# Performance work log

Hardware: AMD Instinct MI355X
Metric: run time of the kernel (lower is better)

## Reference

```python
import jax, jax.numpy as jnp
import numpy as np

B, T, V, E, H = 1024, 256, 90, 8, 256


def setup_inputs() -> dict:
    key = jax.random.key(0)
    ks = jax.random.split(key, 40)
    rn = lambda k, shape: jax.random.normal(k, shape, dtype=jnp.float32) * 0.05
    inp = {}
    inp["input_seq"] = jax.random.randint(ks[0], (B, T), 0, V, dtype=jnp.int32)
    inp["emb"] = rn(ks[1], (V, E)).at[0].set(0.0)  # padding_idx=0
    i = 2
    for name, din in [("g1", E), ("g2", H), ("l1", E), ("l2", H)]:
        inp[name + "_Wih"] = rn(ks[i], (4 * H, din)); i += 1
        inp[name + "_Whh"] = rn(ks[i], (4 * H, H)); i += 1
        inp[name + "_bih"] = rn(ks[i], (4 * H,)); i += 1
        inp[name + "_bhh"] = rn(ks[i], (4 * H,)); i += 1
    for name in ["p1", "p2"]:
        inp[name + "_W1"] = rn(ks[i], (2 * H, E + 4 * H)); i += 1
        inp[name + "_b1"] = rn(ks[i], (2 * H,)); i += 1
        inp[name + "_W2"] = rn(ks[i], (H, 2 * H)); i += 1
        inp[name + "_b2"] = rn(ks[i], (H,)); i += 1
        inp[name + "_W3"] = rn(ks[i], (2, H)); i += 1
        inp[name + "_b3"] = rn(ks[i], (2,)); i += 1
    inp["gfc_W"] = rn(ks[i], (V, H)); i += 1
    inp["gfc_b"] = rn(ks[i], (V,)); i += 1
    inp["lfc_W"] = rn(ks[i], (V, H)); i += 1
    inp["lfc_b"] = rn(ks[i], (V,))
    return inp


def _cell(x, h, c, Wih, Whh, bih, bhh):
    # PyTorch LSTMCell: gate order i, f, g, o
    g = x @ Wih.T + h @ Whh.T + (bih + bhh)
    i, f, gg, o = jnp.split(g, 4, axis=-1)
    c = jax.nn.sigmoid(f) * c + jax.nn.sigmoid(i) * jnp.tanh(gg)
    return jax.nn.sigmoid(o) * jnp.tanh(c), c


def _mlp(x, W1, b1, W2, b2, W3, b3):
    h = jax.nn.relu(x @ W1.T + b1)
    h = jax.nn.relu(h @ W2.T + b2)
    return h @ W3.T + b3


def _forward(input_seq, emb,
             g1_Wih, g1_Whh, g1_bih, g1_bhh, g2_Wih, g2_Whh, g2_bih, g2_bhh,
             l1_Wih, l1_Whh, l1_bih, l1_bhh, l2_Wih, l2_Whh, l2_bih, l2_bhh,
             p1_W1, p1_b1, p1_W2, p1_b2, p1_W3, p1_b3,
             p2_W1, p2_b1, p2_W2, p2_b2, p2_W3, p2_b3,
             gfc_W, gfc_b, lfc_W, lfc_b):
    Bn = input_seq.shape[0]
    embeds = emb[input_seq]  # [B, T, E]
    z = jnp.zeros((Bn, H), dtype=emb.dtype)

    def step(carry, e):
        gh1, gc1, gh2, gc2, lh1, lc1, lh2, lc2 = carry
        gh1, gc1 = _cell(e, gh1, gc1, g1_Wih, g1_Whh, g1_bih, g1_bhh)
        lh1, lc1 = _cell(e, lh1, lc1, l1_Wih, l1_Whh, l1_bih, l1_bhh)
        p = jax.nn.softmax(_mlp(jnp.concatenate([e, gh1, gc1, lh1, lc1], 1),
                                p1_W1, p1_b1, p1_W2, p1_b2, p1_W3, p1_b3), axis=1)
        # bmm([B,1,2],[B,2,H]) == p0*local + p1*global
        gh1 = p[:, 0:1] * lh1 + p[:, 1:2] * gh1
        gc1 = p[:, 0:1] * lc1 + p[:, 1:2] * gc1
        gh2, gc2 = _cell(gh1, gh2, gc2, g2_Wih, g2_Whh, g2_bih, g2_bhh)
        lh2, lc2 = _cell(lh1, lh2, lc2, l2_Wih, l2_Whh, l2_bih, l2_bhh)
        p = jax.nn.softmax(_mlp(jnp.concatenate([e, gh2, gc2, lh2, lc2], 1),
                                p2_W1, p2_b1, p2_W2, p2_b2, p2_W3, p2_b3), axis=1)
        gh2 = p[:, 0:1] * lh2 + p[:, 1:2] * gh2
        gc2 = p[:, 0:1] * lc2 + p[:, 1:2] * gc2
        return (gh1, gc1, gh2, gc2, lh1, lc1, lh2, lc2), gh2

    _, hs = jax.lax.scan(step, (z, z, z, z, z, z, z, z), jnp.swapaxes(embeds, 0, 1))
    hs = jnp.swapaxes(hs, 0, 1)  # [B, T, H]
    out = 0.5 * (hs @ gfc_W.T + gfc_b) + 0.5 * (hs @ lfc_W.T + lfc_b)
    return jnp.swapaxes(out, 1, 2)  # [B, V, T]


def reference(input_seq, emb,
              g1_Wih, g1_Whh, g1_bih, g1_bhh, g2_Wih, g2_Whh, g2_bih, g2_bhh,
              l1_Wih, l1_Whh, l1_bih, l1_bhh, l2_Wih, l2_Whh, l2_bih, l2_bhh,
              p1_W1, p1_b1, p1_W2, p1_b2, p1_W3, p1_b3,
              p2_W1, p2_b1, p2_W2, p2_b2, p2_W3, p2_b3,
              gfc_W, gfc_b, lfc_W, lfc_b):
    return _forward(input_seq, emb,
                    g1_Wih, g1_Whh, g1_bih, g1_bhh, g2_Wih, g2_Whh, g2_bih, g2_bhh,
                    l1_Wih, l1_Whh, l1_bih, l1_bhh, l2_Wih, l2_Whh, l2_bih, l2_bhh,
                    p1_W1, p1_b1, p1_W2, p1_b2, p1_W3, p1_b3,
                    p2_W1, p2_b1, p2_W2, p2_b2, p2_W3, p2_b3,
                    gfc_W, gfc_b, lfc_W, lfc_b)
```

## Files before the change

kernel.cpp:

```cpp
#include <hip/hip_runtime.h>

#define B_ 1024
#define T_ 256
#define V_ 90
#define H_ 256
#define NTHR 512
#define NBLK 256
#define S_ (B_*H_)

constexpr size_t OFF_GH1C = 0;
constexpr size_t OFF_GC1C = OFF_GH1C + S_;
constexpr size_t OFF_GH1P = OFF_GC1C + S_;
constexpr size_t OFF_GC1P = OFF_GH1P + S_;
constexpr size_t OFF_LH1  = OFF_GC1P + S_;
constexpr size_t OFF_LC1  = OFF_LH1 + 2*S_;
constexpr size_t OFF_GH2C = OFF_LC1 + 2*S_;
constexpr size_t OFF_GC2C = OFF_GH2C + S_;
constexpr size_t OFF_GH2P = OFF_GC2C + S_;
constexpr size_t OFF_GC2P = OFF_GH2P + S_;
constexpr size_t OFF_LH2  = OFF_GC2P + S_;
constexpr size_t OFF_LC2  = OFF_LH2 + 2*S_;
constexpr size_t OFF_MLP1 = OFF_LC2 + 2*S_;
constexpr size_t OFF_EX   = OFF_MLP1 + (size_t)B_*512;
constexpr size_t OFF_WG1  = OFF_EX + 2*B_*8;
constexpr size_t OFF_WE1  = OFF_WG1 + 256*2048;
constexpr size_t OFF_BG1  = OFF_WE1 + 8*2048;
constexpr size_t OFF_WL2  = OFF_BG1 + 2048;
constexpr size_t OFF_BL2  = OFF_WL2 + 512*1024;
constexpr size_t OFF_WG2  = OFF_BL2 + 1024;
constexpr size_t OFF_BG2  = OFF_WG2 + 512*1024;
constexpr size_t OFF_WP1  = OFF_BG2 + 1024;
constexpr size_t OFF_WEP1 = OFF_WP1 + 1024*512;
constexpr size_t OFF_WP2  = OFF_WEP1 + 8*512;
constexpr size_t OFF_WEP2 = OFF_WP2 + 1024*512;
constexpr size_t OFF_WB1  = OFF_WEP2 + 8*512;
constexpr size_t OFF_WB2  = OFF_WB1 + 512*256;
constexpr size_t OFF_WOUT = OFF_WB2 + 512*256;
constexpr size_t OFF_BOUT = OFF_WOUT + 256*96;
constexpr size_t OFF_BAR  = OFF_BOUT + 112;
constexpr size_t WS_FLOATS = OFF_BAR + 8192;

struct InP {
  const int*   seq;
  const float* emb;
  const float *g1_Wih,*g1_Whh,*g1_bih,*g1_bhh;
  const float *g2_Wih,*g2_Whh,*g2_bih,*g2_bhh;
  const float *l1_Wih,*l1_Whh,*l1_bih,*l1_bhh;
  const float *l2_Wih,*l2_Whh,*l2_bih,*l2_bhh;
  const float *p1_W1,*p1_b1,*p1_W2,*p1_b2,*p1_W3,*p1_b3;
  const float *p2_W1,*p2_b1,*p2_W2,*p2_b2,*p2_W3,*p2_b3;
  const float *gfc_W,*gfc_b,*lfc_W,*lfc_b;
};

__device__ __forceinline__ float sig_(float x)  { return 1.f/(1.f+__expf(-x)); }
__device__ __forceinline__ float tanh_(float x) { return 1.f - 2.f/(__expf(2.f*x)+1.f); }

__device__ __forceinline__ unsigned ld_flag(const unsigned* p) {
  unsigned v;
  asm volatile("global_load_dword %0, %1, off sc1\n\ts_waitcnt vmcnt(0)"
               : "=v"(v) : "v"(p) : "memory");
  return v;
}
__device__ __forceinline__ void st_flag(unsigned* p, unsigned v) {
  asm volatile("global_store_dword %0, %1, off sc1\n\ts_waitcnt vmcnt(0)"
               :: "v"(p), "v"(v) : "memory");
}

__device__ __forceinline__ void gbar_x(unsigned* arr, unsigned* go, int slot, unsigned ep)
{
  __syncthreads();
  if (threadIdx.x < 64) {
    if (threadIdx.x == 0) st_flag(&arr[slot*16], ep);
    if (slot == 0) {
      if (threadIdx.x < 32) {
        int cap = 0;
        for (;;) {
          unsigned v = ld_flag(&arr[threadIdx.x*16]);
          if (v >= ep) break;
          __builtin_amdgcn_s_sleep(2);
          if (++cap > 65536) break;
        }
      }
      if (threadIdx.x == 0) st_flag(go, ep);
    } else if (threadIdx.x == 0) {
      int cap = 0;
      for (;;) {
        unsigned v = ld_flag(go);
        if (v >= ep) break;
        __builtin_amdgcn_s_sleep(2);
        if (++cap > 65536) break;
      }
    }
  }
  __syncthreads();
  asm volatile("buffer_inv sc0" ::: "memory");
}

template<int CT, int TR, int NSEG, bool HASE, class FE>
__device__ __forceinline__ void mm_tile(
    float* sAb, float* sWb, float* sWe, float* sE,
    const float* s0, const float* s1_, const float* s2_, const float* s3_,
    const float* Wm, int ldw, int ct0,
    const float* We, int ldwe, const float* ex,
    int r0, FE fe)
{
  constexpr int NTX = CT / 4;
  constexpr int LDW = CT + 4;
  constexpr int K   = NSEG * 256;
  constexpr int NC  = K / 32;
  constexpr int WPT = (32*CT)/NTHR;
  const int tid = threadIdx.x;
  const int tx = tid % NTX, ty = tid / NTX;
  const int ar = tid >> 3, ak = (tid & 7) << 2;
  const int kkw = tid >> 4, cw = (tid & 15) * WPT;

  if (HASE) {
    for (int i = tid; i < 8*CT; i += NTHR) {
      int kk = i / CT, c = i - kk*CT;
      sWe[kk*LDW + c] = We[(size_t)kk*ldwe + ct0 + c];
    }
    sE[tid] = ex[((r0 + (tid>>3))<<3) + (tid & 7)];
  }

  float acc[TR][4];
#pragma unroll
  for (int i = 0; i < TR; ++i)
#pragma unroll
    for (int j = 0; j < 4; ++j) acc[i][j] = 0.f;

  auto lda = [&](int k0) -> float4 {
    const float* S;
    if (NSEG == 1) S = s0;
    else if (NSEG == 2) S = (k0 < 256) ? s0 : s1_;
    else S = (k0 < 256) ? s0 : (k0 < 512) ? s1_ : (k0 < 768) ? s2_ : s3_;
    return *(const float4*)&S[(size_t)(r0 + ar)*H_ + (k0 & 255) + ak];
  };
  auto ldwv0 = [&](int k0) { return *(const float4*)&Wm[(size_t)(k0 + kkw)*ldw + ct0 + cw]; };
  auto ldwv1 = [&](int k0) { return *(const float4*)&Wm[(size_t)(k0 + kkw)*ldw + ct0 + cw + 4]; };

  auto storec = [&](int pb, const float4& pa, const float4& pw0, const float4& pw1) {
    float* a = sAb + pb*2176;
    a[(ak+0)*68 + ar] = pa.x; a[(ak+1)*68 + ar] = pa.y;
    a[(ak+2)*68 + ar] = pa.z; a[(ak+3)*68 + ar] = pa.w;
    float* w = sWb + pb*4224 + kkw*LDW + cw;
    *(float4*)w = pw0;
    if (WPT == 8) *(float4*)(w+4) = pw1;
  };

  auto compute = [&](const float* a, const float* w) {
#pragma unroll 8
    for (int kk = 0; kk < 32; ++kk) {
      float4 wv = *(const float4*)&w[kk*LDW + tx*4];
      if constexpr (TR == 4) {
        float4 av = *(const float4*)&a[kk*68 + ty*4];
        float avv[4] = {av.x, av.y, av.z, av.w};
#pragma unroll
        for (int i = 0; i < 4; ++i) {
          acc[i][0] = __builtin_fmaf(avv[i], wv.x, acc[i][0]);
          acc[i][1] = __builtin_fmaf(avv[i], wv.y, acc[i][1]);
          acc[i][2] = __builtin_fmaf(avv[i], wv.z, acc[i][2]);
          acc[i][3] = __builtin_fmaf(avv[i], wv.w, acc[i][3]);
        }
      } else {
        float2 av = *(const float2*)&a[kk*68 + ty*2];
        float avv[2] = {av.x, av.y};
#pragma unroll
        for (int i = 0; i < 2; ++i) {
          acc[i][0] = __builtin_fmaf(avv[i], wv.x, acc[i][0]);
          acc[i][1] = __builtin_fmaf(avv[i], wv.y, acc[i][1]);
          acc[i][2] = __builtin_fmaf(avv[i], wv.z, acc[i][2]);
          acc[i][3] = __builtin_fmaf(avv[i], wv.w, acc[i][3]);
        }
      }
    }
  };

  float4 pa0, pw00, pw01, pa1, pw10, pw11;
  pa0 = lda(0);  pw00 = ldwv0(0);  if (WPT == 8) pw01 = ldwv1(0);
  pa1 = lda(32); pw10 = ldwv0(32); if (WPT == 8) pw11 = ldwv1(32);
  storec(0, pa0, pw00, pw01);
  __syncthreads();

  for (int c = 0; c < NC; c += 2) {
    if (c + 2 < NC) { pa0 = lda((c+2)*32); pw00 = ldwv0((c+2)*32); if (WPT == 8) pw01 = ldwv1((c+2)*32); }
    compute(sAb, sWb);
    storec(1, pa1, pw10, pw11);
    __syncthreads();
    if (c + 3 < NC) { pa1 = lda((c+3)*32); pw10 = ldwv0((c+3)*32); if (WPT == 8) pw11 = ldwv1((c+3)*32); }
    compute(sAb + 2176, sWb + 4224);
    if (c + 2 < NC) storec(0, pa0, pw00, pw01);
    __syncthreads();
  }

  if (HASE) {
#pragma unroll
    for (int j = 0; j < 8; ++j) {
      float4 wv = *(const float4*)&sWe[j*LDW + tx*4];
#pragma unroll
      for (int i = 0; i < TR; ++i) {
        float ev = sE[(ty*TR + i)*8 + j];
        acc[i][0] = __builtin_fmaf(ev, wv.x, acc[i][0]);
        acc[i][1] = __builtin_fmaf(ev, wv.y, acc[i][1]);
        acc[i][2] = __builtin_fmaf(ev, wv.z, acc[i][2]);
        acc[i][3] = __builtin_fmaf(ev, wv.w, acc[i][3]);
      }
    }
  }
  fe(tx, ty, acc);
}

__device__ __forceinline__ void stage_F2(
    int rowbase,
    const float* mlp1, const float* WB, const float* b2,
    const float* W3, const float* b3,
    const float* lh, const float* lc,
    const float* ghp, const float* gcp,
    float* ghc, float* gcc)
{
  const int w = threadIdx.x >> 6, lane = threadIdx.x & 63;
  const int r0 = rowbase + w*2;
  const float* a0 = mlp1 + (size_t)r0*512;
  const float* a1 = a0 + 512;
  float m0[4] = {0.f,0.f,0.f,0.f}, m1[4] = {0.f,0.f,0.f,0.f};
  for (int k0 = 0; k0 < 512; k0 += 4) {
    float4 x0 = *(const float4*)&a0[k0];
    float4 x1 = *(const float4*)&a1[k0];
    float xv0[4] = {x0.x,x0.y,x0.z,x0.w};
    float xv1[4] = {x1.x,x1.y,x1.z,x1.w};
#pragma unroll
    for (int j = 0; j < 4; ++j) {
      float4 wv = *(const float4*)&WB[(size_t)(k0+j)*256 + lane*4];
      m0[0] = __builtin_fmaf(xv0[j], wv.x, m0[0]);
      m0[1] = __builtin_fmaf(xv0[j], wv.y, m0[1]);
      m0[2] = __builtin_fmaf(xv0[j], wv.z, m0[2]);
      m0[3] = __builtin_fmaf(xv0[j], wv.w, m0[3]);
      m1[0] = __builtin_fmaf(xv1[j], wv.x, m1[0]);
      m1[1] = __builtin_fmaf(xv1[j], wv.y, m1[1]);
      m1[2] = __builtin_fmaf(xv1[j], wv.z, m1[2]);
      m1[3] = __builtin_fmaf(xv1[j], wv.w, m1[3]);
    }
  }
  float4 b = *(const float4*)&b2[lane*4];
  float bb[4] = {b.x,b.y,b.z,b.w};
#pragma unroll
  for (int j = 0; j < 4; ++j) {
    m0[j] = fmaxf(m0[j]+bb[j], 0.f);
    m1[j] = fmaxf(m1[j]+bb[j], 0.f);
  }
  float4 w30 = *(const float4*)&W3[lane*4];
  float4 w31 = *(const float4*)&W3[256 + lane*4];
  float w0v[4] = {w30.x,w30.y,w30.z,w30.w};
  float w1v[4] = {w31.x,w31.y,w31.z,w31.w};
  float d00=0.f, d01=0.f, d10=0.f, d11=0.f;
#pragma unroll
  for (int j = 0; j < 4; ++j) {
    d00 = __builtin_fmaf(m0[j], w0v[j], d00);
    d01 = __builtin_fmaf(m0[j], w1v[j], d01);
    d10 = __builtin_fmaf(m1[j], w0v[j], d10);
    d11 = __builtin_fmaf(m1[j], w1v[j], d11);
  }
#pragma unroll
  for (int off = 32; off; off >>= 1) {
    d00 += __shfl_xor(d00, off, 64); d01 += __shfl_xor(d01, off, 64);
    d10 += __shfl_xor(d10, off, 64); d11 += __shfl_xor(d11, off, 64);
  }
  d00 += b3[0]; d01 += b3[1]; d10 += b3[0]; d11 += b3[1];
  float mxa = fmaxf(d00, d01), mxb = fmaxf(d10, d11);
  float e00 = __expf(d00-mxa), e01 = __expf(d01-mxa);
  float e10 = __expf(d10-mxb), e11 = __expf(d11-mxb);
  float ia = 1.f/(e00+e01), ib = 1.f/(e10+e11);
  float p0a = e00*ia, p1a = e01*ia;
  float p0b = e10*ib, p1b = e11*ib;
#pragma unroll
  for (int rr = 0; rr < 2; ++rr) {
    const float p0 = rr ? p0b : p0a, p1 = rr ? p1b : p1a;
    const size_t ix = (size_t)(r0+rr)*H_ + lane*4;
    float4 lv = *(const float4*)&lh[ix];
    float4 gv = *(const float4*)&ghp[ix];
    float4 o;
    o.x = p0*lv.x + p1*gv.x; o.y = p0*lv.y + p1*gv.y;
    o.z = p0*lv.z + p1*gv.z; o.w = p0*lv.w + p1*gv.w;
    *(float4*)&ghc[ix] = o;
    lv = *(const float4*)&lc[ix];
    gv = *(const float4*)&gcp[ix];
    o.x = p0*lv.x + p1*gv.x; o.y = p0*lv.y + p1*gv.y;
    o.z = p0*lv.z + p1*gv.z; o.w = p0*lv.w + p1*gv.w;
    *(float4*)&gcc[ix] = o;
  }
}

__device__ __forceinline__ void stage_OUT(
    const float* gh2c, const float* WOUT, const float* BOUT,
    float* out, int rbase, int tt)
{
  const int w = threadIdx.x >> 6, lane = threadIdx.x & 63;
  const int r = rbase + w;
  const float* arow = gh2c + (size_t)r * H_;
  float acc0 = 0.f, acc1 = 0.f;
  const bool two = lane < (V_ - 64);
  for (int k0 = 0; k0 < 256; k0 += 4) {
    float4 a4 = *(const float4*)&arow[k0];
    float av[4] = {a4.x, a4.y, a4.z, a4.w};
#pragma unroll
    for (int j = 0; j < 4; ++j) {
      const float* wr = &WOUT[(size_t)(k0+j)*96];
      acc0 = __builtin_fmaf(av[j], wr[lane], acc0);
      if (two) acc1 = __builtin_fmaf(av[j], wr[64+lane], acc1);
    }
  }
  out[((size_t)r*V_ + lane)*T_ + tt] = acc0 + BOUT[lane];
  if (two) out[((size_t)r*V_ + 64 + lane)*T_ + tt] = acc1 + BOUT[64+lane];
}

template<int TR>
struct GateEpi {
  const float* cin; float* ho; float* co; const float* bias; int r0; int hbase;
  __device__ void operator()(int tx, int ty, float (&acc)[TR][4]) const {
    const int h = hbase + tx;
    const float b0 = bias[tx*4+0], b1 = bias[tx*4+1];
    const float b2 = bias[tx*4+2], b3 = bias[tx*4+3];
#pragma unroll
    for (int i = 0; i < TR; ++i) {
      const int r = r0 + ty*TR + i;
      const size_t ix = (size_t)r*H_ + h;
      float gi = sig_(acc[i][0]+b0), gf = sig_(acc[i][1]+b1);
      float gg = tanh_(acc[i][2]+b2), go = sig_(acc[i][3]+b3);
      float cn = gf*cin[ix] + gi*gg;
      ho[ix] = go*tanh_(cn); co[ix] = cn;
    }
  }
};

struct MlpEpi {
  float* mlp1; const float* b1; int r0; int c0;
  __device__ void operator()(int tx, int ty, float (&acc)[2][4]) const {
    const float4 b = *(const float4*)&b1[c0 + tx*4];
#pragma unroll
    for (int i = 0; i < 2; ++i) {
      const int r = r0 + ty*2 + i;
      float4 o;
      o.x = fmaxf(acc[i][0]+b.x, 0.f); o.y = fmaxf(acc[i][1]+b.y, 0.f);
      o.z = fmaxf(acc[i][2]+b.z, 0.f); o.w = fmaxf(acc[i][3]+b.w, 0.f);
      *(float4*)&mlp1[(size_t)r*512 + c0 + tx*4] = o;
    }
  }
};

__global__ void k_setup(InP in, float* __restrict__ ws)
{
  const size_t nthr = (size_t)gridDim.x * blockDim.x;
  const size_t t0 = (size_t)blockIdx.x * blockDim.x + threadIdx.x;

  for (size_t i = t0; i < 16*(size_t)S_; i += nthr) ws[i] = 0.f;
  for (size_t i = t0; i < 8192; i += nthr) ((unsigned*)(ws + OFF_BAR))[i] = 0u;

  for (size_t i = t0; i < (size_t)B_*8; i += nthr) {
    int r = (int)(i >> 3), j = (int)(i & 7);
    ws[OFF_EX + i] = in.emb[(size_t)in.seq[(size_t)r*T_]*8 + j];
  }
  for (size_t i = t0; i < (size_t)256*2048; i += nthr) {
    int k = (int)(i >> 11), n = (int)(i & 2047);
    int cell = n >> 10, nn = n & 1023, h = nn >> 2, g = nn & 3, row = g*256 + h;
    const float* W = cell ? in.l1_Whh : in.g1_Whh;
    ws[OFF_WG1 + i] = W[(size_t)row*256 + k];
  }
  for (size_t i = t0; i < (size_t)8*2048; i += nthr) {
    int k = (int)(i >> 11), n = (int)(i & 2047);
    int cell = n >> 10, nn = n & 1023, h = nn >> 2, g = nn & 3, row = g*256 + h;
    const float* W = cell ? in.l1_Wih : in.g1_Wih;
    ws[OFF_WE1 + i] = W[(size_t)row*8 + k];
  }
  for (size_t i = t0; i < 2048; i += nthr) {
    int cell = (int)(i >> 10), nn = (int)(i & 1023), h = nn >> 2, g = nn & 3, row = g*256 + h;
    ws[OFF_BG1 + i] = cell ? (in.l1_bih[row] + in.l1_bhh[row]) : (in.g1_bih[row] + in.g1_bhh[row]);
  }
  for (size_t i = t0; i < (size_t)2*512*1024; i += nthr) {
    int cell = (int)(i / (512*1024));
    int idx = (int)(i - (size_t)cell*512*1024);
    int k = idx >> 10, n = idx & 1023, h = n >> 2, g = n & 3, row = g*256 + h;
    const float* Wih = cell ? in.l2_Wih : in.g2_Wih;
    const float* Whh = cell ? in.l2_Whh : in.g2_Whh;
    float v = (k < 256) ? Wih[(size_t)row*256 + k] : Whh[(size_t)row*256 + (k-256)];
    ws[(cell ? OFF_WL2 : OFF_WG2) + idx] = v;
  }
  for (size_t i = t0; i < 2048; i += nthr) {
    int cell = (int)(i >> 10), n = (int)(i & 1023), h = n >> 2, g = n & 3, row = g*256 + h;
    float v = cell ? (in.l2_bih[row] + in.l2_bhh[row]) : (in.g2_bih[row] + in.g2_bhh[row]);
    ws[(cell ? OFF_BL2 : OFF_BG2) + n] = v;
  }
  for (size_t i = t0; i < (size_t)2*1024*512; i += nthr) {
    int which = (int)(i / (1024*512));
    int idx = (int)(i - (size_t)which*1024*512);
    int k = idx >> 9, n = idx & 511;
    const float* W = which ? in.p2_W1 : in.p1_W1;
    ws[(which ? OFF_WP2 : OFF_WP1) + idx] = W[(size_t)n*1032 + 8 + k];
  }
  for (size_t i = t0; i < (size_t)2*8*512; i += nthr) {
    int which = (int)(i / (8*512));
    int idx = (int)(i - (size_t)which*8*512);
    int k = idx >> 9, n = idx & 511;
    const float* W = which ? in.p2_W1 : in.p1_W1;
    ws[(which ? OFF_WEP2 : OFF_WEP1) + idx] = W[(size_t)n*1032 + k];
  }
  for (size_t i = t0; i < (size_t)2*512*256; i += nthr) {
    int which = (int)(i / (512*256));
    int idx = (int)(i - (size_t)which*512*256);
    int k = idx >> 8, n = idx & 255;
    const float* W = which ? in.p2_W2 : in.p1_W2;
    ws[(which ? OFF_WB2 : OFF_WB1) + idx] = W[(size_t)n*512 + k];
  }
  for (size_t i = t0; i < (size_t)256*96; i += nthr) {
    int k = (int)(i / 96), c = (int)(i - (size_t)k*96);
    float v = 0.f;
    if (c < V_) v = 0.5f*(in.gfc_W[(size_t)c*256 + k] + in.lfc_W[(size_t)c*256 + k]);
    ws[OFF_WOUT + i] = v;
  }
  for (size_t i = t0; i < 96; i += nthr)
    ws[OFF_BOUT + i] = (i < V_) ? 0.5f*(in.gfc_b[i] + in.lfc_b[i]) : 0.f;
}

__global__ __launch_bounds__(NTHR) void k_main(InP in, float* ws, float* __restrict__ out)
{
  __shared__ __attribute__((aligned(16))) float sA[2*2176];
  __shared__ __attribute__((aligned(16))) float sW[2*4224];
  __shared__ __attribute__((aligned(16))) float sWe[8*132];
  __shared__ __attribute__((aligned(16))) float sE[512];

  float* GH1C = ws + OFF_GH1C;  float* GC1C = ws + OFF_GC1C;
  float* GH1P = ws + OFF_GH1P;  float* GC1P = ws + OFF_GC1P;
  float* LH1  = ws + OFF_LH1;   float* LC1  = ws + OFF_LC1;
  float* GH2C = ws + OFF_GH2C;  float* GC2C = ws + OFF_GC2C;
  float* GH2P = ws + OFF_GH2P;  float* GC2P = ws + OFF_GC2P;
  float* LH2  = ws + OFF_LH2;   float* LC2  = ws + OFF_LC2;
  float* MLP1 = ws + OFF_MLP1;  float* EXB  = ws + OFF_EX;
  const float* WG1 = ws + OFF_WG1;  const float* WE1 = ws + OFF_WE1;  const float* BG1 = ws + OFF_BG1;
  const float* WL2 = ws + OFF_WL2;  const float* BL2 = ws + OFF_BL2;
  const float* WG2 = ws + OFF_WG2;  const float* BG2 = ws + OFF_BG2;
  const float* WP1 = ws + OFF_WP1;  const float* WEP1 = ws + OFF_WEP1;
  const float* WP2 = ws + OFF_WP2;  const float* WEP2 = ws + OFF_WEP2;
  const float* WB1 = ws + OFF_WB1;  const float* WB2 = ws + OFF_WB2;
  const float* WOUT = ws + OFF_WOUT; const float* BOUT = ws + OFF_BOUT;

  unsigned xcc;
  asm volatile("s_getreg_b32 %0, hwreg(HW_REG_XCC_ID)" : "=s"(xcc));
  xcc &= 7u;
  unsigned* barx = ((unsigned*)(ws + OFF_BAR)) + xcc*1024;
  unsigned* arr  = barx;
  unsigned* go   = barx + 512;
  unsigned* reg  = barx + 544;
  __shared__ unsigned s_slot;
  if (threadIdx.x == 0)
    s_slot = __hip_atomic_fetch_add(reg, 1u, __ATOMIC_RELAXED, __HIP_MEMORY_SCOPE_AGENT);
  __syncthreads();
  const int slot  = (int)(s_slot & 31u);
  const int rows0 = (int)xcc * 128;
  unsigned ep = 0;

  for (int t = 0; t < T_; ++t) {
    const int sel = t & 1;
    const float* ex = EXB + sel*(B_*8);
    float* lh1o = LH1 + sel*S_;      float* lh1n = LH1 + (sel^1)*S_;
    float* lc1o = LC1 + sel*S_;      float* lc1n = LC1 + (sel^1)*S_;
    float* lh2o = LH2 + sel*S_;      float* lh2n = LH2 + (sel^1)*S_;
    float* lc2o = LC2 + sel*S_;      float* lc2n = LC2 + (sel^1)*S_;

    {
      const int rt = slot & 1, ct = slot >> 1;
      const int r0 = rows0 + rt*64, ct0 = ct*128;
      const int cell = ct >> 3;
      GateEpi<4> epi{ cell ? lc1o : GC1C,
                      cell ? lh1n : GH1P,
                      cell ? lc1n : GC1P,
                      BG1 + ct0, r0, (ct0 & 1023) >> 2 };
      mm_tile<128,4,1,true>(sA, sW, sWe, sE,
                            cell ? lh1o : GH1C, nullptr, nullptr, nullptr,
                            WG1, 2048, ct0, WE1, 2048, ex, r0, epi);
    }
    gbar_x(arr, go, slot, ++ep);

    if (slot < 16) {
      const int rt = slot & 1, ct = slot >> 1;
      const int r0 = rows0 + rt*64, c0 = ct*64;
      MlpEpi epi{ MLP1, in.p1_b1, r0, c0 };
      mm_tile<64,2,4,true>(sA, sW, sWe, sE,
                           GH1P, GC1P, lh1n, lc1n,
                           WP1, 512, c0, WEP1, 512, ex, r0, epi);
    } else {
      const int s2 = slot - 16;
      const int rt = s2 & 1, ct = s2 >> 1;
      const int r0 = rows0 + rt*64, ct0 = ct*128;
      GateEpi<4> epi{ lc2o, lh2n, lc2n, BL2 + ct0, r0, ct0 >> 2 };
      mm_tile<128,4,2,false>(sA, sW, sWe, sE,
                             lh1n, lh2o, nullptr, nullptr,
                             WL2, 1024, ct0, nullptr, 0, nullptr, r0, epi);
    }
    gbar_x(arr, go, slot, ++ep);

    if (slot < 8) {
      stage_F2(rows0 + slot*16, MLP1, WB1, in.p1_b2, in.p1_W3, in.p1_b3,
               lh1n, lc1n, GH1P, GC1P, GH1C, GC1C);
    } else if (slot < 10 && t < T_-1) {
      const int rb = rows0 + (slot-8)*64;
      const int r = rb + (threadIdx.x >> 3), j = threadIdx.x & 7;
      EXB[((t+1)&1)*(B_*8) + r*8 + j] = in.emb[(size_t)in.seq[(size_t)r*T_ + t + 1]*8 + j];
    }
    gbar_x(arr, go, slot, ++ep);

    {
      const int rt = slot & 1, ct = slot >> 1;
      const int r0 = rows0 + rt*64, ct0 = ct*64;
      GateEpi<2> epi{ GC2C, GH2P, GC2P, BG2 + ct0, r0, ct0 >> 2 };
      mm_tile<64,2,2,false>(sA, sW, sWe, sE,
                            GH1C, GH2C, nullptr, nullptr,
                            WG2, 1024, ct0, nullptr, 0, nullptr, r0, epi);
    }
    gbar_x(arr, go, slot, ++ep);

    if (slot < 16) {
      const int rt = slot & 1, ct = slot >> 1;
      const int r0 = rows0 + rt*64, c0 = ct*64;
      MlpEpi epi{ MLP1, in.p2_b1, r0, c0 };
      mm_tile<64,2,4,true>(sA, sW, sWe, sE,
                           GH2P, GC2P, lh2n, lc2n,
                           WP2, 512, c0, WEP2, 512, ex, r0, epi);
    } else if (t > 0) {
      stage_OUT(GH2C, WOUT, BOUT, out, rows0 + (slot-16)*8, t-1);
    }
    gbar_x(arr, go, slot, ++ep);

    if (slot < 8) {
      stage_F2(rows0 + slot*16, MLP1, WB2, in.p2_b2, in.p2_W3, in.p2_b3,
               lh2n, lc2n, GH2P, GC2P, GH2C, GC2C);
    }
    gbar_x(arr, go, slot, ++ep);
  }

  if (slot >= 16) stage_OUT(GH2C, WOUT, BOUT, out, rows0 + (slot-16)*8, 255);
}

extern "C" void kernel_launch(void* const* d_in, const int* in_sizes, int n_in,
                              void* d_out, int out_size, void* d_ws, size_t ws_size,
                              hipStream_t stream)
{
  if (ws_size < WS_FLOATS * sizeof(float)) return;

  InP in;
  in.seq    = (const int*)  d_in[0];
  in.emb    = (const float*)d_in[1];
  in.g1_Wih = (const float*)d_in[2];  in.g1_Whh = (const float*)d_in[3];
  in.g1_bih = (const float*)d_in[4];  in.g1_bhh = (const float*)d_in[5];
  in.g2_Wih = (const float*)d_in[6];  in.g2_Whh = (const float*)d_in[7];
  in.g2_bih = (const float*)d_in[8];  in.g2_bhh = (const float*)d_in[9];
  in.l1_Wih = (const float*)d_in[10]; in.l1_Whh = (const float*)d_in[11];
  in.l1_bih = (const float*)d_in[12]; in.l1_bhh = (const float*)d_in[13];
  in.l2_Wih = (const float*)d_in[14]; in.l2_Whh = (const float*)d_in[15];
  in.l2_bih = (const float*)d_in[16]; in.l2_bhh = (const float*)d_in[17];
  in.p1_W1  = (const float*)d_in[18]; in.p1_b1  = (const float*)d_in[19];
  in.p1_W2  = (const float*)d_in[20]; in.p1_b2  = (const float*)d_in[21];
  in.p1_W3  = (const float*)d_in[22]; in.p1_b3  = (const float*)d_in[23];
  in.p2_W1  = (const float*)d_in[24]; in.p2_b1  = (const float*)d_in[25];
  in.p2_W2  = (const float*)d_in[26]; in.p2_b2  = (const float*)d_in[27];
  in.p2_W3  = (const float*)d_in[28]; in.p2_b3  = (const float*)d_in[29];
  in.gfc_W  = (const float*)d_in[30]; in.gfc_b  = (const float*)d_in[31];
  in.lfc_W  = (const float*)d_in[32]; in.lfc_b  = (const float*)d_in[33];

  float* ws  = (float*)d_ws;
  float* out = (float*)d_out;

  k_setup<<<256, 256, 0, stream>>>(in, ws);
  k_main <<<NBLK, NTHR, 28672, stream>>>(in, ws, out);
}
```

Before: 64.14 ms.

## Replace scalar FP32 GEMM tiles with split-bf16 MFMA matmuls

Replaces the FMA-based shared-memory GEMM tiles in the persistent LSTM kernel with MFMA 16x16x32 bf16 instructions. Each operand is split into high and low bf16 parts and three products are summed to keep roughly FP32 accuracy. Weights are pre-packed into MFMA fragment layout in setup. The MLP first layer is split across K into two partial buffers, with bias and ReLU moved into stage_F2, and the G2 gate matmul tiling is reshaped to 128-column tiles. This trades extra MFMA work and conversion overhead for much higher matrix throughput, with some risk of precision loss.

Measured after the change: 81.34 ms. 26.8% more time.

```diff
diff --git a/kernel.cpp b/kernel.cpp
--- a/kernel.cpp
+++ b/kernel.cpp
@@ -1,4 +1,5 @@
 #include <hip/hip_runtime.h>
+#include <hip/hip_bf16.h>
 
 #define B_ 1024
 #define T_ 256
@@ -8,36 +9,43 @@
 #define NBLK 256
 #define S_ (B_*H_)
 
-constexpr size_t OFF_GH1C = 0;
-constexpr size_t OFF_GC1C = OFF_GH1C + S_;
-constexpr size_t OFF_GH1P = OFF_GC1C + S_;
-constexpr size_t OFF_GC1P = OFF_GH1P + S_;
-constexpr size_t OFF_LH1  = OFF_GC1P + S_;
-constexpr size_t OFF_LC1  = OFF_LH1 + 2*S_;
-constexpr size_t OFF_GH2C = OFF_LC1 + 2*S_;
-constexpr size_t OFF_GC2C = OFF_GH2C + S_;
-constexpr size_t OFF_GH2P = OFF_GC2C + S_;
-constexpr size_t OFF_GC2P = OFF_GH2P + S_;
-constexpr size_t OFF_LH2  = OFF_GC2P + S_;
-constexpr size_t OFF_LC2  = OFF_LH2 + 2*S_;
-constexpr size_t OFF_MLP1 = OFF_LC2 + 2*S_;
-constexpr size_t OFF_EX   = OFF_MLP1 + (size_t)B_*512;
-constexpr size_t OFF_WG1  = OFF_EX + 2*B_*8;
-constexpr size_t OFF_WE1  = OFF_WG1 + 256*2048;
-constexpr size_t OFF_BG1  = OFF_WE1 + 8*2048;
-constexpr size_t OFF_WL2  = OFF_BG1 + 2048;
-constexpr size_t OFF_BL2  = OFF_WL2 + 512*1024;
-constexpr size_t OFF_WG2  = OFF_BL2 + 1024;
-constexpr size_t OFF_BG2  = OFF_WG2 + 512*1024;
-constexpr size_t OFF_WP1  = OFF_BG2 + 1024;
-constexpr size_t OFF_WEP1 = OFF_WP1 + 1024*512;
-constexpr size_t OFF_WP2  = OFF_WEP1 + 8*512;
-constexpr size_t OFF_WEP2 = OFF_WP2 + 1024*512;
-constexpr size_t OFF_WB1  = OFF_WEP2 + 8*512;
-constexpr size_t OFF_WB2  = OFF_WB1 + 512*256;
-constexpr size_t OFF_WOUT = OFF_WB2 + 512*256;
-constexpr size_t OFF_BOUT = OFF_WOUT + 256*96;
-constexpr size_t OFF_BAR  = OFF_BOUT + 112;
+typedef unsigned short u16;
+typedef __attribute__((ext_vector_type(8))) short bf16x8;
+typedef __attribute__((ext_vector_type(4))) float f32x4;
+typedef __attribute__((ext_vector_type(4))) unsigned short u16x4;
+
+constexpr size_t OFF_GH1C  = 0;
+constexpr size_t OFF_GC1C  = OFF_GH1C + S_;
+constexpr size_t OFF_GH1P  = OFF_GC1C + S_;
+constexpr size_t OFF_GC1P  = OFF_GH1P + S_;
+constexpr size_t OFF_LH1   = OFF_GC1P + S_;
+constexpr size_t OFF_LC1   = OFF_LH1 + 2*S_;
+constexpr size_t OFF_GH2C  = OFF_LC1 + 2*S_;
+constexpr size_t OFF_GC2C  = OFF_GH2C + S_;
+constexpr size_t OFF_GH2P  = OFF_GC2C + S_;
+constexpr size_t OFF_GC2P  = OFF_GH2P + S_;
+constexpr size_t OFF_LH2   = OFF_GC2P + S_;
+constexpr size_t OFF_LC2   = OFF_LH2 + 2*S_;
+constexpr size_t OFF_MLP1A = OFF_LC2 + 2*S_;
+constexpr size_t OFF_MLP1B = OFF_MLP1A + (size_t)B_*512;
+constexpr size_t OFF_EX    = OFF_MLP1B + (size_t)B_*512;
+constexpr size_t OFF_WG1PK = OFF_EX + 2*B_*8;
+constexpr size_t OFF_WE1   = OFF_WG1PK + 256*2048/1*1;
+constexpr size_t OFF_WE1_  = OFF_WG1PK + (size_t)256*2048;
+constexpr size_t OFF_BG1   = OFF_WE1_ + 8*2048;
+constexpr size_t OFF_WL2PK = OFF_BG1 + 2048;
+constexpr size_t OFF_BL2   = OFF_WL2PK + (size_t)512*1024;
+constexpr size_t OFF_WG2PK = OFF_BL2 + 1024;
+constexpr size_t OFF_BG2   = OFF_WG2PK + (size_t)512*1024;
+constexpr size_t OFF_WP1PK = OFF_BG2 + 1024;
+constexpr size_t OFF_WEP1  = OFF_WP1PK + (size_t)1024*512;
+constexpr size_t OFF_WP2PK = OFF_WEP1 + 8*512;
+constexpr size_t OFF_WEP2  = OFF_WP2PK + (size_t)1024*512;
+constexpr size_t OFF_WB1   = OFF_WEP2 + 8*512;
+constexpr size_t OFF_WB2   = OFF_WB1 + 512*256;
+constexpr size_t OFF_WOUT  = OFF_WB2 + 512*256;
+constexpr size_t OFF_BOUT  = OFF_WOUT + 256*96;
+constexpr size_t OFF_BAR   = OFF_BOUT + 128;
 constexpr size_t WS_FLOATS = OFF_BAR + 8192;
 
 struct InP {
@@ -54,6 +62,15 @@
 
 __device__ __forceinline__ float sig_(float x)  { return 1.f/(1.f+__expf(-x)); }
 __device__ __forceinline__ float tanh_(float x) { return 1.f - 2.f/(__expf(2.f*x)+1.f); }
+
+__device__ __forceinline__ unsigned short f2bf(float v) {
+  unsigned u = __builtin_bit_cast(unsigned, v);
+  u += 0x7FFFu + ((u >> 16) & 1u);
+  return (unsigned short)(u >> 16);
+}
+__device__ __forceinline__ float bf2f(unsigned short s) {
+  unsigned u = (unsigned)s << 16; return __builtin_bit_cast(float, u);
+}
 
 __device__ __forceinline__ unsigned ld_flag(const unsigned* p) {
   unsigned v;
@@ -96,122 +113,144 @@
   asm volatile("buffer_inv sc0" ::: "memory");
 }
 
-template<int CT, int TR, int NSEG, bool HASE, class FE>
-__device__ __forceinline__ void mm_tile(
-    float* sAb, float* sWb, float* sWe, float* sE,
-    const float* s0, const float* s1_, const float* s2_, const float* s3_,
-    const float* Wm, int ldw, int ct0,
-    const float* We, int ldwe, const float* ex,
-    int r0, FE fe)
+template<int NCH, int NSEG, bool HASE, class FE>
+__device__ __forceinline__ void mm_mfma(
+    u16* sAB, float* sWe, float* sE,
+    const float* s0, const float* s1_,
+    const u16* Wpk, int wstep,
+    const float* WeP, int ldwe, const float* ex,
+    int r0, int ct0, FE fe)
 {
-  constexpr int NTX = CT / 4;
-  constexpr int LDW = CT + 4;
-  constexpr int K   = NSEG * 256;
-  constexpr int NC  = K / 32;
-  constexpr int WPT = (32*CT)/NTHR;
+  constexpr int BUFU = 12288;
   const int tid = threadIdx.x;
-  const int tx = tid % NTX, ty = tid / NTX;
+  const int lane = tid & 63;
+  const int wr = (tid >> 6) & 3, wc = tid >> 8;
   const int ar = tid >> 3, ak = (tid & 7) << 2;
-  const int kkw = tid >> 4, cw = (tid & 15) * WPT;
 
   if (HASE) {
-    for (int i = tid; i < 8*CT; i += NTHR) {
-      int kk = i / CT, c = i - kk*CT;
-      sWe[kk*LDW + c] = We[(size_t)kk*ldwe + ct0 + c];
-    }
-    sE[tid] = ex[((r0 + (tid>>3))<<3) + (tid & 7)];
-  }
-
-  float acc[TR][4];
-#pragma unroll
-  for (int i = 0; i < TR; ++i)
-#pragma unroll
-    for (int j = 0; j < 4; ++j) acc[i][j] = 0.f;
-
-  auto lda = [&](int k0) -> float4 {
-    const float* S;
-    if (NSEG == 1) S = s0;
-    else if (NSEG == 2) S = (k0 < 256) ? s0 : s1_;
-    else S = (k0 < 256) ? s0 : (k0 < 512) ? s1_ : (k0 < 768) ? s2_ : s3_;
-    return *(const float4*)&S[(size_t)(r0 + ar)*H_ + (k0 & 255) + ak];
+    for (int i = tid; i < 8*128; i += NTHR)
+      sWe[i] = WeP[(i >> 7) * ldwe + ct0 + (i & 127)];
+    sE[tid] = ex[((r0 + ar) << 3) + (tid & 7)];
+  }
+
+  f32x4 acc[4] = {{0,0,0,0},{0,0,0,0},{0,0,0,0},{0,0,0,0}};
+
+  auto lda = [&](int c) -> float4 {
+    int k0 = c * 32;
+    const float* S = (NSEG == 1) ? s0 : ((k0 < 256) ? s0 : s1_);
+    return *(const float4*)&S[(size_t)(r0 + ar) * H_ + (k0 & 255) + ak];
   };
-  auto ldwv0 = [&](int k0) { return *(const float4*)&Wm[(size_t)(k0 + kkw)*ldw + ct0 + cw]; };
-  auto ldwv1 = [&](int k0) { return *(const float4*)&Wm[(size_t)(k0 + kkw)*ldw + ct0 + cw + 4]; };
-
-  auto storec = [&](int pb, const float4& pa, const float4& pw0, const float4& pw1) {
-    float* a = sAb + pb*2176;
-    a[(ak+0)*68 + ar] = pa.x; a[(ak+1)*68 + ar] = pa.y;
-    a[(ak+2)*68 + ar] = pa.z; a[(ak+3)*68 + ar] = pa.w;
-    float* w = sWb + pb*4224 + kkw*LDW + cw;
-    *(float4*)w = pw0;
-    if (WPT == 8) *(float4*)(w+4) = pw1;
+  auto ldw = [&](int c, float4& w0, float4& w1) {
+    const float* p = (const float*)(Wpk + (size_t)c * wstep) + tid * 8;
+    w0 = *(const float4*)p; w1 = *(const float4*)(p + 4);
   };
-
-  auto compute = [&](const float* a, const float* w) {
-#pragma unroll 8
-    for (int kk = 0; kk < 32; ++kk) {
-      float4 wv = *(const float4*)&w[kk*LDW + tx*4];
-      if constexpr (TR == 4) {
-        float4 av = *(const float4*)&a[kk*68 + ty*4];
-        float avv[4] = {av.x, av.y, av.z, av.w};
-#pragma unroll
-        for (int i = 0; i < 4; ++i) {
-          acc[i][0] = __builtin_fmaf(avv[i], wv.x, acc[i][0]);
-          acc[i][1] = __builtin_fmaf(avv[i], wv.y, acc[i][1]);
-          acc[i][2] = __builtin_fmaf(avv[i], wv.z, acc[i][2]);
-          acc[i][3] = __builtin_fmaf(avv[i], wv.w, acc[i][3]);
-        }
-      } else {
-        float2 av = *(const float2*)&a[kk*68 + ty*2];
-        float avv[2] = {av.x, av.y};
-#pragma unroll
-        for (int i = 0; i < 2; ++i) {
-          acc[i][0] = __builtin_fmaf(avv[i], wv.x, acc[i][0]);
-          acc[i][1] = __builtin_fmaf(avv[i], wv.y, acc[i][1]);
-          acc[i][2] = __builtin_fmaf(avv[i], wv.z, acc[i][2]);
-          acc[i][3] = __builtin_fmaf(avv[i], wv.w, acc[i][3]);
-        }
-      }
-    }
+  auto storec = [&](int pb, const float4& pa, const float4& w0, const float4& w1) {
+    float vv[4] = {pa.x, pa.y, pa.z, pa.w};
+    u16x4 hv, lv;
+#pragma unroll
+    for (int j = 0; j < 4; ++j) {
+      unsigned short hb = f2bf(vv[j]);
+      hv[j] = hb;
+      lv[j] = f2bf(vv[j] - bf2f(hb));
+    }
+    u16* base = sAB + pb*BUFU;
+    const int aoff = (ar >> 4)*512 + ((ar & 15) + ((ak >> 3) << 4))*8 + (ak & 7);
+    *(u16x4*)(base + aoff) = hv;
+    *(u16x4*)(base + 2048 + aoff) = lv;
+    float* wb = (float*)(base + 4096) + tid*8;
+    *(float4*)wb = w0; *(float4*)(wb + 4) = w1;
   };
-
-  float4 pa0, pw00, pw01, pa1, pw10, pw11;
-  pa0 = lda(0);  pw00 = ldwv0(0);  if (WPT == 8) pw01 = ldwv1(0);
-  pa1 = lda(32); pw10 = ldwv0(32); if (WPT == 8) pw11 = ldwv1(32);
+  auto compute = [&](int pb) {
+    u16* base = sAB + pb*BUFU;
+    const u16* Ap = base + wr*512 + lane*8;
+    bf16x8 a_hi = *(const bf16x8*)Ap;
+    bf16x8 a_lo = *(const bf16x8*)(Ap + 2048);
+    const u16* Bp = base + 4096 + (wc*4)*1024 + lane*8;
+#pragma unroll
+    for (int t = 0; t < 4; ++t) {
+      bf16x8 b_hi = *(const bf16x8*)(Bp + t*1024);
+      bf16x8 b_lo = *(const bf16x8*)(Bp + t*1024 + 512);
+      acc[t] = __builtin_amdgcn_mfma_f32_16x16x32_bf16(a_hi, b_hi, acc[t], 0, 0, 0);
+      acc[t] = __builtin_amdgcn_mfma_f32_16x16x32_bf16(a_lo, b_hi, acc[t], 0, 0, 0);
+      acc[t] = __builtin_amdgcn_mfma_f32_16x16x32_bf16(a_hi, b_lo, acc[t], 0, 0, 0);
+    }
+  };
+
+  float4 pa0, pa1, pw00, pw01, pw10, pw11;
+  pa0 = lda(0); ldw(0, pw00, pw01);
+  pa1 = lda(1); ldw(1, pw10, pw11);
   storec(0, pa0, pw00, pw01);
   __syncthreads();
-
-  for (int c = 0; c < NC; c += 2) {
-    if (c + 2 < NC) { pa0 = lda((c+2)*32); pw00 = ldwv0((c+2)*32); if (WPT == 8) pw01 = ldwv1((c+2)*32); }
-    compute(sAb, sWb);
+  for (int c = 0; c < NCH; c += 2) {
+    if (c + 2 < NCH) { pa0 = lda(c+2); ldw(c+2, pw00, pw01); }
+    compute(0);
     storec(1, pa1, pw10, pw11);
     __syncthreads();
-    if (c + 3 < NC) { pa1 = lda((c+3)*32); pw10 = ldwv0((c+3)*32); if (WPT == 8) pw11 = ldwv1((c+3)*32); }
-    compute(sAb + 2176, sWb + 4224);
-    if (c + 2 < NC) storec(0, pa0, pw00, pw01);
+    if (c + 3 < NCH) { pa1 = lda(c+3); ldw(c+3, pw10, pw11); }
+    compute(1);
+    if (c + 2 < NCH) storec(0, pa0, pw00, pw01);
     __syncthreads();
   }
 
   if (HASE) {
 #pragma unroll
-    for (int j = 0; j < 8; ++j) {
-      float4 wv = *(const float4*)&sWe[j*LDW + tx*4];
-#pragma unroll
-      for (int i = 0; i < TR; ++i) {
-        float ev = sE[(ty*TR + i)*8 + j];
-        acc[i][0] = __builtin_fmaf(ev, wv.x, acc[i][0]);
-        acc[i][1] = __builtin_fmaf(ev, wv.y, acc[i][1]);
-        acc[i][2] = __builtin_fmaf(ev, wv.z, acc[i][2]);
-        acc[i][3] = __builtin_fmaf(ev, wv.w, acc[i][3]);
+    for (int t = 0; t < 4; ++t) {
+      const int colL = wc*64 + t*16 + (lane & 15);
+      float w[8];
+#pragma unroll
+      for (int j = 0; j < 8; ++j) w[j] = sWe[j*128 + colL];
+#pragma unroll
+      for (int m = 0; m < 4; ++m) {
+        const int rr = wr*16 + ((lane >> 4) << 2) + m;
+        float s = 0.f;
+#pragma unroll
+        for (int j = 0; j < 8; ++j) s = __builtin_fmaf(sE[rr*8 + j], w[j], s);
+        acc[t][m] += s;
       }
     }
   }
-  fe(tx, ty, acc);
-}
+  fe(wr, wc, lane, acc);
+}
+
+struct GateEpiM {
+  const float* cin; float* ho; float* co; const float* bias_pk;
+  int r0; int ct0; int hb0;
+  __device__ void operator()(int wr, int wc, int lane, f32x4 (&acc)[4]) const {
+    const int h = hb0 + wc*16 + (lane & 15);
+    const int rbase = r0 + wr*16 + ((lane >> 4) << 2);
+    float b[4];
+#pragma unroll
+    for (int t = 0; t < 4; ++t) b[t] = bias_pk[ct0 + wc*64 + t*16 + (lane & 15)];
+#pragma unroll
+    for (int m = 0; m < 4; ++m) {
+      const size_t ix = (size_t)(rbase + m)*H_ + h;
+      float gi = sig_(acc[0][m] + b[0]);
+      float gf = sig_(acc[1][m] + b[1]);
+      float gg = tanh_(acc[2][m] + b[2]);
+      float go = sig_(acc[3][m] + b[3]);
+      float cn = gf*cin[ix] + gi*gg;
+      ho[ix] = go*tanh_(cn); co[ix] = cn;
+    }
+  }
+};
+
+struct MlpEpiM {
+  float* dst; int r0; int ct0;
+  __device__ void operator()(int wr, int wc, int lane, f32x4 (&acc)[4]) const {
+    const int rbase = r0 + wr*16 + ((lane >> 4) << 2);
+    const int c0 = ct0 + wc*64 + (lane & 15);
+#pragma unroll
+    for (int t = 0; t < 4; ++t)
+#pragma unroll
+      for (int m = 0; m < 4; ++m)
+        dst[(size_t)(rbase + m)*512 + c0 + t*16] = acc[t][m];
+  }
+};
 
 __device__ __forceinline__ void stage_F2(
     int rowbase,
-    const float* mlp1, const float* WB, const float* b2,
+    const float* mlpA, const float* mlpB, const float* b1,
+    const float* WB, const float* b2,
     const float* W3, const float* b3,
     const float* lh, const float* lc,
     const float* ghp, const float* gcp,
@@ -219,14 +258,19 @@
 {
   const int w = threadIdx.x >> 6, lane = threadIdx.x & 63;
   const int r0 = rowbase + w*2;
-  const float* a0 = mlp1 + (size_t)r0*512;
-  const float* a1 = a0 + 512;
+  const float* aA0 = mlpA + (size_t)r0*512; const float* aB0 = mlpB + (size_t)r0*512;
+  const float* aA1 = aA0 + 512;             const float* aB1 = aB0 + 512;
   float m0[4] = {0.f,0.f,0.f,0.f}, m1[4] = {0.f,0.f,0.f,0.f};
   for (int k0 = 0; k0 < 512; k0 += 4) {
-    float4 x0 = *(const float4*)&a0[k0];
-    float4 x1 = *(const float4*)&a1[k0];
-    float xv0[4] = {x0.x,x0.y,x0.z,x0.w};
-    float xv1[4] = {x1.x,x1.y,x1.z,x1.w};
+    float4 xa = *(const float4*)&aA0[k0];
+    float4 xb = *(const float4*)&aB0[k0];
+    float4 ya = *(const float4*)&aA1[k0];
+    float4 yb = *(const float4*)&aB1[k0];
+    float4 bb = *(const float4*)&b1[k0];
+    float xv0[4] = { fmaxf(xa.x+xb.x+bb.x,0.f), fmaxf(xa.y+xb.y+bb.y,0.f),
+                     fmaxf(xa.z+xb.z+bb.z,0.f), fmaxf(xa.w+xb.w+bb.w,0.f) };
+    float xv1[4] = { fmaxf(ya.x+yb.x+bb.x,0.f), fmaxf(ya.y+yb.y+bb.y,0.f),
+                     fmaxf(ya.z+yb.z+bb.z,0.f), fmaxf(ya.w+yb.w+bb.w,0.f) };
 #pragma unroll
     for (int j = 0; j < 4; ++j) {
       float4 wv = *(const float4*)&WB[(size_t)(k0+j)*256 + lane*4];
@@ -241,11 +285,11 @@
     }
   }
   float4 b = *(const float4*)&b2[lane*4];
-  float bb[4] = {b.x,b.y,b.z,b.w};
+  float bb2[4] = {b.x,b.y,b.z,b.w};
 #pragma unroll
   for (int j = 0; j < 4; ++j) {
-    m0[j] = fmaxf(m0[j]+bb[j], 0.f);
-    m1[j] = fmaxf(m1[j]+bb[j], 0.f);
+    m0[j] = fmaxf(m0[j]+bb2[j], 0.f);
+    m1[j] = fmaxf(m1[j]+bb2[j], 0.f);
   }
   float4 w30 = *(const float4*)&W3[lane*4];
   float4 w31 = *(const float4*)&W3[256 + lane*4];
@@ -303,48 +347,14 @@
     float av[4] = {a4.x, a4.y, a4.z, a4.w};
 #pragma unroll
     for (int j = 0; j < 4; ++j) {
-      const float* wr = &WOUT[(size_t)(k0+j)*96];
-      acc0 = __builtin_fmaf(av[j], wr[lane], acc0);
-      if (two) acc1 = __builtin_fmaf(av[j], wr[64+lane], acc1);
+      const float* wr_ = &WOUT[(size_t)(k0+j)*96];
+      acc0 = __builtin_fmaf(av[j], wr_[lane], acc0);
+      if (two) acc1 = __builtin_fmaf(av[j], wr_[64+lane], acc1);
     }
   }
   out[((size_t)r*V_ + lane)*T_ + tt] = acc0 + BOUT[lane];
   if (two) out[((size_t)r*V_ + 64 + lane)*T_ + tt] = acc1 + BOUT[64+lane];
 }
-
-template<int TR>
-struct GateEpi {
-  const float* cin; float* ho; float* co; const float* bias; int r0; int hbase;
-  __device__ void operator()(int tx, int ty, float (&acc)[TR][4]) const {
-    const int h = hbase + tx;
-    const float b0 = bias[tx*4+0], b1 = bias[tx*4+1];
-    const float b2 = bias[tx*4+2], b3 = bias[tx*4+3];
-#pragma unroll
-    for (int i = 0; i < TR; ++i) {
-      const int r = r0 + ty*TR + i;
-      const size_t ix = (size_t)r*H_ + h;
-      float gi = sig_(acc[i][0]+b0), gf = sig_(acc[i][1]+b1);
-      float gg = tanh_(acc[i][2]+b2), go = sig_(acc[i][3]+b3);
-      float cn = gf*cin[ix] + gi*gg;
-      ho[ix] = go*tanh_(cn); co[ix] = cn;
-    }
-  }
-};
-
-struct MlpEpi {
-  float* mlp1; const float* b1; int r0; int c0;
-  __device__ void operator()(int tx, int ty, float (&acc)[2][4]) const {
-    const float4 b = *(const float4*)&b1[c0 + tx*4];
-#pragma unroll
-    for (int i = 0; i < 2; ++i) {
-      const int r = r0 + ty*2 + i;
-      float4 o;
-      o.x = fmaxf(acc[i][0]+b.x, 0.f); o.y = fmaxf(acc[i][1]+b.y, 0.f);
-      o.z = fmaxf(acc[i][2]+b.z, 0.f); o.w = fmaxf(acc[i][3]+b.w, 0.f);
-      *(float4*)&mlp1[(size_t)r*512 + c0 + tx*4] = o;
-    }
-  }
-};
 
 __global__ void k_setup(InP in, float* __restrict__ ws)
 {
@@ -358,50 +368,79 @@
     int r = (int)(i >> 3), j = (int)(i & 7);
     ws[OFF_EX + i] = in.emb[(size_t)in.seq[(size_t)r*T_]*8 + j];
   }
-  for (size_t i = t0; i < (size_t)256*2048; i += nthr) {
-    int k = (int)(i >> 11), n = (int)(i & 2047);
-    int cell = n >> 10, nn = n & 1023, h = nn >> 2, g = nn & 3, row = g*256 + h;
-    const float* W = cell ? in.l1_Whh : in.g1_Whh;
-    ws[OFF_WG1 + i] = W[(size_t)row*256 + k];
+
+  {
+    u16* dst = (u16*)(ws + OFF_WG1PK);
+    for (size_t i = t0; i < (size_t)8*128*512; i += nthr) {
+      int e = (int)(i & 7), lane = (int)((i >> 3) & 63);
+      int tile = (int)((i >> 9) & 127), ck = (int)(i >> 16);
+      int p = tile*16 + (lane & 15);
+      int k = ck*32 + ((lane >> 4) << 3) + e;
+      int cell = p >> 10, q = p & 1023;
+      int h = ((q >> 6) << 4) + (q & 15), g = (q >> 4) & 3, R = g*256 + h;
+      float w = (cell ? in.l1_Whh : in.g1_Whh)[(size_t)R*256 + k];
+      unsigned short hb = f2bf(w), lb = f2bf(w - bf2f(hb));
+      size_t o = ((size_t)(ck*128 + tile)*2)*512 + lane*8 + e;
+      dst[o] = hb; dst[o + 512] = lb;
+    }
   }
   for (size_t i = t0; i < (size_t)8*2048; i += nthr) {
-    int k = (int)(i >> 11), n = (int)(i & 2047);
-    int cell = n >> 10, nn = n & 1023, h = nn >> 2, g = nn & 3, row = g*256 + h;
-    const float* W = cell ? in.l1_Wih : in.g1_Wih;
-    ws[OFF_WE1 + i] = W[(size_t)row*8 + k];
+    int j = (int)(i >> 11), p = (int)(i & 2047);
+    int cell = p >> 10, q = p & 1023;
+    int h = ((q >> 6) << 4) + (q & 15), g = (q >> 4) & 3, R = g*256 + h;
+    ws[OFF_WE1_ + (size_t)j*2048 + p] = (cell ? in.l1_Wih : in.g1_Wih)[(size_t)R*8 + j];
   }
   for (size_t i = t0; i < 2048; i += nthr) {
-    int cell = (int)(i >> 10), nn = (int)(i & 1023), h = nn >> 2, g = nn & 3, row = g*256 + h;
-    ws[OFF_BG1 + i] = cell ? (in.l1_bih[row] + in.l1_bhh[row]) : (in.g1_bih[row] + in.g1_bhh[row]);
-  }
-  for (size_t i = t0; i < (size_t)2*512*1024; i += nthr) {
-    int cell = (int)(i / (512*1024));
-    int idx = (int)(i - (size_t)cell*512*1024);
-    int k = idx >> 10, n = idx & 1023, h = n >> 2, g = n & 3, row = g*256 + h;
-    const float* Wih = cell ? in.l2_Wih : in.g2_Wih;
-    const float* Whh = cell ? in.l2_Whh : in.g2_Whh;
-    float v = (k < 256) ? Wih[(size_t)row*256 + k] : Whh[(size_t)row*256 + (k-256)];
-    ws[(cell ? OFF_WL2 : OFF_WG2) + idx] = v;
-  }
-  for (size_t i = t0; i < 2048; i += nthr) {
-    int cell = (int)(i >> 10), n = (int)(i & 1023), h = n >> 2, g = n & 3, row = g*256 + h;
-    float v = cell ? (in.l2_bih[row] + in.l2_bhh[row]) : (in.g2_bih[row] + in.g2_bhh[row]);
-    ws[(cell ? OFF_BL2 : OFF_BG2) + n] = v;
-  }
-  for (size_t i = t0; i < (size_t)2*1024*512; i += nthr) {
-    int which = (int)(i / (1024*512));
-    int idx = (int)(i - (size_t)which*1024*512);
-    int k = idx >> 9, n = idx & 511;
+    int p = (int)i, cell = p >> 10, q = p & 1023;
+    int h = ((q >> 6) << 4) + (q & 15), g = (q >> 4) & 3, R = g*256 + h;
+    ws[OFF_BG1 + i] = cell ? (in.l1_bih[R] + in.l1_bhh[R]) : (in.g1_bih[R] + in.g1_bhh[R]);
+  }
+
+  for (int which = 0; which < 2; ++which) {
+    u16* dst = (u16*)(ws + (which ? OFF_WG2PK : OFF_WL2PK));
+    const float* Wih = which ? in.g2_Wih : in.l2_Wih;
+    const float* Whh = which ? in.g2_Whh : in.l2_Whh;
+    for (size_t i = t0; i < (size_t)16*64*512; i += nthr) {
+      int e = (int)(i & 7), lane = (int)((i >> 3) & 63);
+      int tile = (int)((i >> 9) & 63), ck = (int)(i >> 15);
+      int p = tile*16 + (lane & 15);
+      int k = ck*32 + ((lane >> 4) << 3) + e;
+      int h = ((p >> 6) << 4) + (p & 15), g = (p >> 4) & 3, R = g*256 + h;
+      float w = (k < 256) ? Wih[(size_t)R*256 + k] : Whh[(size_t)R*256 + (k-256)];
+      unsigned short hb = f2bf(w), lb = f2bf(w - bf2f(hb));
+      size_t o = ((size_t)(ck*64 + tile)*2)*512 + lane*8 + e;
+      dst[o] = hb; dst[o + 512] = lb;
+    }
+  }
+  for (size_t i = t0; i < 2*1024; i += nthr) {
+    int which = (int)(i >> 10), p = (int)(i & 1023);
+    int h = ((p >> 6) << 4) + (p & 15), g = (p >> 4) & 3, R = g*256 + h;
+    float v = which ? (in.g2_bih[R] + in.g2_bhh[R]) : (in.l2_bih[R] + in.l2_bhh[R]);
+    ws[(which ? OFF_BG2 : OFF_BL2) + p] = v;
+  }
+
+  for (int which = 0; which < 2; ++which) {
+    u16* dst = (u16*)(ws + (which ? OFF_WP2PK : OFF_WP1PK));
     const float* W = which ? in.p2_W1 : in.p1_W1;
-    ws[(which ? OFF_WP2 : OFF_WP1) + idx] = W[(size_t)n*1032 + 8 + k];
+    for (size_t i = t0; i < (size_t)32*32*512; i += nthr) {
+      int e = (int)(i & 7), lane = (int)((i >> 3) & 63);
+      int tile = (int)((i >> 9) & 31), ck = (int)(i >> 14);
+      int p = tile*16 + (lane & 15);
+      int k = ck*32 + ((lane >> 4) << 3) + e;
+      float w = W[(size_t)p*1032 + 8 + k];
+      unsigned short hb = f2bf(w), lb = f2bf(w - bf2f(hb));
+      size_t o = ((size_t)(ck*32 + tile)*2)*512 + lane*8 + e;
+      dst[o] = hb; dst[o + 512] = lb;
+    }
   }
   for (size_t i = t0; i < (size_t)2*8*512; i += nthr) {
     int which = (int)(i / (8*512));
     int idx = (int)(i - (size_t)which*8*512);
-    int k = idx >> 9, n = idx & 511;
+    int j = idx >> 9, p = idx & 511;
     const float* W = which ? in.p2_W1 : in.p1_W1;
-    ws[(which ? OFF_WEP2 : OFF_WEP1) + idx] = W[(size_t)n*1032 + k];
-  }
+    ws[(which ? OFF_WEP2 : OFF_WEP1) + (size_t)j*512 + p] = W[(size_t)p*1032 + j];
+  }
+
   for (size_t i = t0; i < (size_t)2*512*256; i += nthr) {
     int which = (int)(i / (512*256));
     int idx = (int)(i - (size_t)which*512*256);
@@ -421,9 +460,8 @@
 
 __global__ __launch_bounds__(NTHR) void k_main(InP in, float* ws, float* __restrict__ out)
 {
-  __shared__ __attribute__((aligned(16))) float sA[2*2176];
-  __shared__ __attribute__((aligned(16))) float sW[2*4224];
-  __shared__ __attribute__((aligned(16))) float sWe[8*132];
+  __shared__ __attribute__((aligned(16))) u16   sAB[2*12288];
+  __shared__ __attribute__((aligned(16))) float sWe[8*128];
   __shared__ __attribute__((aligned(16))) float sE[512];
 
   float* GH1C = ws + OFF_GH1C;  float* GC1C = ws + OFF_GC1C;
@@ -432,13 +470,17 @@
   float* GH2C = ws + OFF_GH2C;  float* GC2C = ws + OFF_GC2C;
   float* GH2P = ws + OFF_GH2P;  float* GC2P = ws + OFF_GC2P;
   float* LH2  = ws + OFF_LH2;   float* LC2  = ws + OFF_LC2;
-  float* MLP1 = ws + OFF_MLP1;  float* EXB  = ws + OFF_EX;
-  const float* WG1 = ws + OFF_WG1;  const float* WE1 = ws + OFF_WE1;  const float* BG1 = ws + OFF_BG1;
-  const float* WL2 = ws + OFF_WL2;  const float* BL2 = ws + OFF_BL2;
-  const float* WG2 = ws + OFF_WG2;  const float* BG2 = ws + OFF_BG2;
-  const float* WP1 = ws + OFF_WP1;  const float* WEP1 = ws + OFF_WEP1;
-  const float* WP2 = ws + OFF_WP2;  const float* WEP2 = ws + OFF_WEP2;
-  const float* WB1 = ws + OFF_WB1;  const float* WB2 = ws + OFF_WB2;
+  float* MLPA = ws + OFF_MLP1A; float* MLPB = ws + OFF_MLP1B;
+  float* EXB  = ws + OFF_EX;
+  const u16* WG1PK = (const u16*)(ws + OFF_WG1PK);
+  const u16* WL2PK = (const u16*)(ws + OFF_WL2PK);
+  const u16* WG2PK = (const u16*)(ws + OFF_WG2PK);
+  const u16* WP1PK = (const u16*)(ws + OFF_WP1PK);
+  const u16* WP2PK = (const u16*)(ws + OFF_WP2PK);
+  const float* WE1 = ws + OFF_WE1_;  const float* BG1P = ws + OFF_BG1;
+  const float* BL2P = ws + OFF_BL2;  const float* BG2P = ws + OFF_BG2;
+  const float* WEP1 = ws + OFF_WEP1; const float* WEP2 = ws + OFF_WEP2;
+  const float* WB1 = ws + OFF_WB1;   const float* WB2 = ws + OFF_WB2;
   const float* WOUT = ws + OFF_WOUT; const float* BOUT = ws + OFF_BOUT;
 
   unsigned xcc;
@@ -468,37 +510,46 @@
       const int rt = slot & 1, ct = slot >> 1;
       const int r0 = rows0 + rt*64, ct0 = ct*128;
       const int cell = ct >> 3;
-      GateEpi<4> epi{ cell ? lc1o : GC1C,
-                      cell ? lh1n : GH1P,
-                      cell ? lc1n : GC1P,
-                      BG1 + ct0, r0, (ct0 & 1023) >> 2 };
-      mm_tile<128,4,1,true>(sA, sW, sWe, sE,
-                            cell ? lh1o : GH1C, nullptr, nullptr, nullptr,
-                            WG1, 2048, ct0, WE1, 2048, ex, r0, epi);
+      GateEpiM epi{ cell ? lc1o : GC1C,
+                    cell ? lh1n : GH1P,
+                    cell ? lc1n : GC1P,
+                    BG1P, r0, ct0, ((ct0 & 1023) >> 6) << 4 };
+      mm_mfma<8, 1, true>(sAB, sWe, sE,
+                          cell ? lh1o : GH1C, nullptr,
+                          WG1PK + (size_t)(ct0 >> 4)*1024, 128*1024,
+                          WE1, 2048, ex, r0, ct0, epi);
     }
     gbar_x(arr, go, slot, ++ep);
 
     if (slot < 16) {
-      const int rt = slot & 1, ct = slot >> 1;
-      const int r0 = rows0 + rt*64, c0 = ct*64;
-      MlpEpi epi{ MLP1, in.p1_b1, r0, c0 };
-      mm_tile<64,2,4,true>(sA, sW, sWe, sE,
-                           GH1P, GC1P, lh1n, lc1n,
-                           WP1, 512, c0, WEP1, 512, ex, r0, epi);
+      const int rt = slot & 1, q = slot >> 1;
+      const int ct = q & 3, kh = q >> 2;
+      const int r0 = rows0 + rt*64, ct0 = ct*128;
+      if (kh == 0) {
+        MlpEpiM epi{ MLPA, r0, ct0 };
+        mm_mfma<16, 2, false>(sAB, sWe, sE, GH1P, GC1P,
+                              WP1PK + (size_t)(ct0 >> 4)*1024, 32*1024,
+                              nullptr, 0, nullptr, r0, ct0, epi);
+      } else {
+        MlpEpiM epi{ MLPB, r0, ct0 };
+        mm_mfma<16, 2, true>(sAB, sWe, sE, lh1n, lc1n,
+                             WP1PK + (size_t)16*32*1024 + (size_t)(ct0 >> 4)*1024, 32*1024,
+                             WEP1, 512, ex, r0, ct0, epi);
+      }
     } else {
       const int s2 = slot - 16;
       const int rt = s2 & 1, ct = s2 >> 1;
       const int r0 = rows0 + rt*64, ct0 = ct*128;
-      GateEpi<4> epi{ lc2o, lh2n, lc2n, BL2 + ct0, r0, ct0 >> 2 };
-      mm_tile<128,4,2,false>(sA, sW, sWe, sE,
-                             lh1n, lh2o, nullptr, nullptr,
-                             WL2, 1024, ct0, nullptr, 0, nullptr, r0, epi);
+      GateEpiM epi{ lc2o, lh2n, lc2n, BL2P, r0, ct0, (ct0 >> 6) << 4 };
+      mm_mfma<16, 2, false>(sAB, sWe, sE, lh1n, lh2o,
+                            WL2PK + (size_t)(ct0 >> 4)*1024, 64*1024,
+                            nullptr, 0, nullptr, r0, ct0, epi);
     }
     gbar_x(arr, go, slot, ++ep);
 
     if (slot < 8) {
-      stage_F2(rows0 + slot*16, MLP1, WB1, in.p1_b2, in.p1_W3, in.p1_b3,
-               lh1n, lc1n, GH1P, GC1P, GH1C, GC1C);
+      stage_F2(rows0 + slot*16, MLPA, MLPB, in.p1_b1, WB1, in.p1_b2,
+               in.p1_W3, in.p1_b3, lh1n, lc1n, GH1P, GC1P, GH1C, GC1C);
     } else if (slot < 10 && t < T_-1) {
       const int rb = rows0 + (slot-8)*64;
       const int r = rb + (threadIdx.x >> 3), j = threadIdx.x & 7;
@@ -506,31 +557,39 @@
     }
     gbar_x(arr, go, slot, ++ep);
 
-    {
-      const int rt = slot & 1, ct = slot >> 1;
-      const int r0 = rows0 + rt*64, ct0 = ct*64;
-      GateEpi<2> epi{ GC2C, GH2P, GC2P, BG2 + ct0, r0, ct0 >> 2 };
-      mm_tile<64,2,2,false>(sA, sW, sWe, sE,
-                            GH1C, GH2C, nullptr, nullptr,
-                            WG2, 1024, ct0, nullptr, 0, nullptr, r0, epi);
-    }
-    gbar_x(arr, go, slot, ++ep);
-
     if (slot < 16) {
       const int rt = slot & 1, ct = slot >> 1;
-      const int r0 = rows0 + rt*64, c0 = ct*64;
-      MlpEpi epi{ MLP1, in.p2_b1, r0, c0 };
-      mm_tile<64,2,4,true>(sA, sW, sWe, sE,
-                           GH2P, GC2P, lh2n, lc2n,
-                           WP2, 512, c0, WEP2, 512, ex, r0, epi);
+      const int r0 = rows0 + rt*64, ct0 = ct*128;
+      GateEpiM epi{ GC2C, GH2P, GC2P, BG2P, r0, ct0, (ct0 >> 6) << 4 };
+      mm_mfma<16, 2, false>(sAB, sWe, sE, GH1C, GH2C,
+                            WG2PK + (size_t)(ct0 >> 4)*1024, 64*1024,
+                            nullptr, 0, nullptr, r0, ct0, epi);
     } else if (t > 0) {
       stage_OUT(GH2C, WOUT, BOUT, out, rows0 + (slot-16)*8, t-1);
     }
     gbar_x(arr, go, slot, ++ep);
 
+    if (slot < 16) {
+      const int rt = slot & 1, q = slot >> 1;
+      const int ct = q & 3, kh = q >> 2;
+      const int r0 = rows0 + rt*64, ct0 = ct*128;
+      if (kh == 0) {
+        MlpEpiM epi{ MLPA, r0, ct0 };
+        mm_mfma<16, 2, false>(sAB, sWe, sE, GH2P, GC2P,
+                              WP2PK + (size_t)(ct0 >> 4)*1024, 32*1024,
+                              nullptr, 0, nullptr, r0, ct0, epi);
+      } else {
+        MlpEpiM epi{ MLPB, r0, ct0 };
+        mm_mfma<16, 2, true>(sAB, sWe, sE, lh2n, lc2n,
+                             WP2PK + (size_t)16*32*1024 + (size_t)(ct0 >> 4)*1024, 32*1024,
+                             WEP2, 512, ex, r0, ct0, epi);
+      }
+    }
+    gbar_x(arr, go, slot, ++ep);
+
     if (slot < 8) {
-      stage_F2(rows0 + slot*16, MLP1, WB2, in.p2_b2, in.p2_W3, in.p2_b3,
-               lh2n, lc2n, GH2P, GC2P, GH2C, GC2C);
+      stage_F2(rows0 + slot*16, MLPA, MLPB, in.p2_b1, WB2, in.p2_b2,
+               in.p2_W3, in.p2_b3, lh2n, lc2n, GH2P, GC2P, GH2C, GC2C);
     }
     gbar_x(arr, go, slot, ++ep);
   }
@@ -567,6 +626,6 @@
   float* ws  = (float*)d_ws;
   float* out = (float*)d_out;
 
-  k_setup<<<256, 256, 0, stream>>>(in, ws);
+  k_setup<<<512, 256, 0, stream>>>(in, ws);
   k_main <<<NBLK, NTHR, 28672, stream>>>(in, ws, out);
 }
```
